# Kernel tuning notes

Measured on AMD Instinct MI355X. Metric: run time of the kernel, lower is better.

The kernel has to match this reference:

```python
import jax, jax.numpy as jnp
import numpy as np

B, S, D, H = 4, 2048, 1024, 16
HD = D // H  # head dim = 64


def setup_inputs() -> dict:
    key = jax.random.key(0)
    ks = jax.random.split(key, 10)
    sd = 1.0 / np.sqrt(D)
    return {
        "x": jax.random.normal(ks[0], (B, S, D), jnp.float32),
        "Wq": jax.random.normal(ks[1], (D, D), jnp.float32) * sd,
        "Wk": jax.random.normal(ks[2], (D, D), jnp.float32) * sd,
        "Wv": jax.random.normal(ks[3], (D, D), jnp.float32) * sd,
        "in_w": jax.random.normal(ks[4], (3 * D, D), jnp.float32) * sd,
        "in_b": jax.random.normal(ks[5], (3 * D,), jnp.float32) * 0.01,
        "out_w": jax.random.normal(ks[6], (D, D), jnp.float32) * sd,
        "out_b": jax.random.normal(ks[7], (D,), jnp.float32) * 0.01,
        "proj_w": jax.random.normal(ks[8], (D, D), jnp.float32) * sd,
        "proj_b": jax.random.normal(ks[9], (D,), jnp.float32) * 0.01,
    }


def _attn_block(x, Wq, Wk, Wv, in_w, in_b, out_w, out_b, proj_w, proj_b):
    b, s, d = x.shape
    # redundant pre-projections (bias-free)
    q = jnp.einsum('bsd,ed->bse', x, Wq)
    k = jnp.einsum('bsd,ed->bse', x, Wk)
    v = jnp.einsum('bsd,ed->bse', x, Wv)
    # MultiheadAttention internal in-projection (with bias)
    wq, wk, wv = in_w[:d], in_w[d:2 * d], in_w[2 * d:]
    bq, bk, bv = in_b[:d], in_b[d:2 * d], in_b[2 * d:]
    Q = jnp.einsum('bse,fe->bsf', q, wq) + bq
    K = jnp.einsum('bse,fe->bsf', k, wk) + bk
    V = jnp.einsum('bse,fe->bsf', v, wv) + bv
    # split heads -> [b, h, s, hd]
    Q = Q.reshape(b, s, H, HD).transpose(0, 2, 1, 3)
    K = K.reshape(b, s, H, HD).transpose(0, 2, 1, 3)
    V = V.reshape(b, s, H, HD).transpose(0, 2, 1, 3)
    scale = 1.0 / np.sqrt(HD)
    scores = jnp.einsum('bhqd,bhkd->bhqk', Q * scale, K)
    # FAITHFUL quirk: float tril mask (ones / zeros) is ADDED to scores,
    # exactly as torch does with a float attn_mask (not a -inf causal mask).
    mask = jnp.tril(jnp.ones((s, s), scores.dtype))
    scores = scores + mask
    A = jax.nn.softmax(scores, axis=-1)
    ctx = jnp.einsum('bhqk,bhkd->bhqd', A, V)
    ctx = ctx.transpose(0, 2, 1, 3).reshape(b, s, d)
    attn = jnp.einsum('bse,fe->bsf', ctx, out_w) + out_b  # out_proj
    out = jnp.einsum('bse,fe->bsf', attn, proj_w) + proj_b  # self.project
    return x + out


def reference(x, Wq, Wk, Wv, in_w, in_b, out_w, out_b, proj_w, proj_b):
    return _attn_block(x, Wq, Wk, Wv, in_w, in_b, out_w, out_b, proj_w, proj_b)
```

## Files before the change

### kernel.cpp

```cpp
#include <hip/hip_runtime.h>
#include <stdint.h>

typedef unsigned short u16;
typedef __attribute__((ext_vector_type(8))) short bfx8;
typedef __attribute__((ext_vector_type(4))) float fx4;
typedef __attribute__((ext_vector_type(16))) float fx16;

static __device__ __forceinline__ u16 f2b(float f) {
  union { float f; uint32_t u; } v; v.f = f;
  uint32_t r = v.u + 0x7fffu + ((v.u >> 16) & 1u);
  return (u16)(r >> 16);
}

static __device__ __forceinline__ uint32_t cvtpk(float lo, float hi) {
  uint32_t r;
  asm("v_cvt_pk_bf16_f32 %0, %1, %2" : "=v"(r) : "v"(lo), "v"(hi));
  return r;
}

static __device__ __forceinline__ float ex2(float x) {
  float r;
  asm("v_exp_f32 %0, %1" : "=v"(r) : "v"(x));
  return r;
}

static __device__ __forceinline__ void gload16(const void* g, void* lds) {
  __builtin_amdgcn_global_load_lds((const __attribute__((address_space(1))) uint32_t*)g,
                                   (__attribute__((address_space(3))) uint32_t*)lds,
                                   16, 0, 0);
}

__global__ __launch_bounds__(256) void f32_to_bf16_k(const float* __restrict__ in,
                                                     u16* __restrict__ out, int n) {
  int i = (blockIdx.x * 256 + threadIdx.x) * 8;
  if (i >= n) return;
  float4 a = *(const float4*)(in + i);
  float4 b = *(const float4*)(in + i + 4);
  bfx8 o;
  o[0]=(short)f2b(a.x); o[1]=(short)f2b(a.y); o[2]=(short)f2b(a.z); o[3]=(short)f2b(a.w);
  o[4]=(short)f2b(b.x); o[5]=(short)f2b(b.y); o[6]=(short)f2b(b.z); o[7]=(short)f2b(b.w);
  *(bfx8*)(out + i) = o;
}

struct TransArgs { const float* in[4]; u16* out[4]; };
__global__ __launch_bounds__(256) void transpose4_k(TransArgs ta) {
  const float* in = ta.in[blockIdx.z];
  u16* out = ta.out[blockIdx.z];
  __shared__ u16 t[64][65];
  const int bx = blockIdx.x * 64, by = blockIdx.y * 64;
  const int tid = threadIdx.x;
#pragma unroll
  for (int i = 0; i < 16; ++i) {
    int idx = tid + i * 256; int r = idx >> 6, c = idx & 63;
    t[c][r] = f2b(in[(size_t)(by + r) * 1024 + bx + c]);
  }
  __syncthreads();
#pragma unroll
  for (int i = 0; i < 16; ++i) {
    int idx = tid + i * 256; int r = idx >> 6, c = idx & 63;
    out[(size_t)(bx + r) * 1024 + by + c] = t[r][c];
  }
}

__global__ __launch_bounds__(256) void make_b2_k(const float* __restrict__ pw,
                                                 const float* __restrict__ ob,
                                                 const float* __restrict__ pb,
                                                 float* __restrict__ b2) {
  const int f = blockIdx.x, tid = threadIdx.x;
  float s = 0.f;
  for (int e = tid; e < 1024; e += 256) s += pw[(size_t)f * 1024 + e] * ob[e];
#pragma unroll
  for (int d = 1; d < 64; d <<= 1) s += __shfl_xor(s, d);
  __shared__ float red[4];
  if ((tid & 63) == 0) red[tid >> 6] = s;
  __syncthreads();
  if (tid == 0) b2[f] = red[0] + red[1] + red[2] + red[3] + pb[f];
}

static __device__ __forceinline__ void gemm_core(const u16* __restrict__ A,
                                                 const u16* __restrict__ Bt,
                                                 int K, int bm, int bn,
                                                 u16* As, u16* Bs, fx4 (&acc)[4][4]) {
  const int tid = threadIdx.x, w = tid >> 6, l = tid & 63, lm = l & 15, lk = l >> 4;
  const int wm = w >> 1, wn = w & 1;
  const int nkt = K >> 6;
  for (int kt = 0; kt < nkt; ++kt) {
#pragma unroll
    for (int i = 0; i < 4; ++i) {
      int off = i * 4096 + w * 1024;
      int loff = off + l * 16;
      int row = loff >> 7, cb = loff & 127;
      gload16((const char*)A + ((size_t)(bm * 128 + row) * K + kt * 64) * 2 + cb,
              (char*)As + off);
      gload16((const char*)Bt + ((size_t)(bn * 128 + row) * K + kt * 64) * 2 + cb,
              (char*)Bs + off);
    }
    __syncthreads();
#pragma unroll
    for (int kk = 0; kk < 2; ++kk) {
      bfx8 a[4], b[4];
#pragma unroll
      for (int mi = 0; mi < 4; ++mi)
        a[mi] = *(const bfx8*)((const char*)As + (wm * 64 + mi * 16 + lm) * 128 + lk * 16 + kk * 64);
#pragma unroll
      for (int nj = 0; nj < 4; ++nj)
        b[nj] = *(const bfx8*)((const char*)Bs + (wn * 64 + nj * 16 + lm) * 128 + lk * 16 + kk * 64);
#pragma unroll
      for (int mi = 0; mi < 4; ++mi)
#pragma unroll
        for (int nj = 0; nj < 4; ++nj)
          acc[mi][nj] = __builtin_amdgcn_mfma_f32_16x16x32_bf16(a[mi], b[nj], acc[mi][nj], 0, 0, 0);
    }
    __syncthreads();
  }
}

struct CombArgs { const u16* A[4]; const u16* Bt[4]; u16* C[4]; };
__global__ __launch_bounds__(256) void gemm_combine_k(CombArgs ca) {
  const int z = blockIdx.z;
  __shared__ u16 As[8192], Bs[8192];
  fx4 acc[4][4];
#pragma unroll
  for (int mi = 0; mi < 4; ++mi)
#pragma unroll
    for (int nj = 0; nj < 4; ++nj) acc[mi][nj] = 0.f;
  gemm_core(ca.A[z], ca.Bt[z], 1024, blockIdx.x, blockIdx.y, As, Bs, acc);
  const int tid = threadIdx.x, w = tid >> 6, l = tid & 63, lm = l & 15, lk = l >> 4;
  const int wm = w >> 1, wn = w & 1;
  u16* C = ca.C[z];
#pragma unroll
  for (int mi = 0; mi < 4; ++mi)
#pragma unroll
    for (int nj = 0; nj < 4; ++nj)
#pragma unroll
      for (int r = 0; r < 4; ++r) {
        int m = blockIdx.x * 128 + wm * 64 + mi * 16 + lk * 4 + r;
        int n = blockIdx.y * 128 + wn * 64 + nj * 16 + lm;
        C[(size_t)m * 1024 + n] = f2b(acc[mi][nj][r]);
      }
}

__global__ __launch_bounds__(256) void gemm_qkv_k(const u16* __restrict__ xb,
                                                  const u16* __restrict__ Wc,
                                                  const float* __restrict__ bias,
                                                  u16* __restrict__ Qh, u16* __restrict__ Kh,
                                                  u16* __restrict__ Vh) {
  __shared__ u16 As[8192], Bs[8192];
  fx4 acc[4][4];
#pragma unroll
  for (int mi = 0; mi < 4; ++mi)
#pragma unroll
    for (int nj = 0; nj < 4; ++nj) acc[mi][nj] = 0.f;
  gemm_core(xb, Wc, 1024, blockIdx.x, blockIdx.y, As, Bs, acc);
  const int tid = threadIdx.x, w = tid >> 6, l = tid & 63, lm = l & 15, lk = l >> 4;
  const int wm = w >> 1, wn = w & 1;
  const int t = (blockIdx.y * 128) >> 10;
  u16* dst = (t == 0) ? Qh : ((t == 1) ? Kh : Vh);
#pragma unroll
  for (int mi = 0; mi < 4; ++mi)
#pragma unroll
    for (int nj = 0; nj < 4; ++nj)
#pragma unroll
      for (int r = 0; r < 4; ++r) {
        int m = blockIdx.x * 128 + wm * 64 + mi * 16 + lk * 4 + r;
        int n = blockIdx.y * 128 + wn * 64 + nj * 16 + lm;
        float v = acc[mi][nj][r] + bias[n];
        int f = n & 1023, h = f >> 6, hd = f & 63, b = m >> 11, s = m & 2047;
        size_t hb = ((size_t)(b * 16 + h)) * 131072;
        size_t idx;
        if (t == 2) {
          int sl = s & 63, st = s >> 6;
          idx = hb + (size_t)st * 4096 + (size_t)(hd * 64 + (sl ^ ((hd & 7) << 3)));
        } else if (t == 1) {
          idx = hb + (size_t)s * 64 + (hd ^ ((s & 7) << 3));
        } else {
          idx = hb + (size_t)s * 64 + hd;
        }
        dst[idx] = f2b(v);
      }
}

__global__ __launch_bounds__(256) void gemm_final_k(const u16* __restrict__ ctx,
                                                    const u16* __restrict__ W2,
                                                    const float* __restrict__ b2,
                                                    const float* __restrict__ x,
                                                    float* __restrict__ out) {
  __shared__ u16 As[8192], Bs[8192];
  fx4 acc[4][4];
#pragma unroll
  for (int mi = 0; mi < 4; ++mi)
#pragma unroll
    for (int nj = 0; nj < 4; ++nj) acc[mi][nj] = 0.f;
  gemm_core(ctx, W2, 1024, blockIdx.x, blockIdx.y, As, Bs, acc);
  const int tid = threadIdx.x, w = tid >> 6, l = tid & 63, lm = l & 15, lk = l >> 4;
  const int wm = w >> 1, wn = w & 1;
#pragma unroll
  for (int mi = 0; mi < 4; ++mi)
#pragma unroll
    for (int nj = 0; nj < 4; ++nj)
#pragma unroll
      for (int r = 0; r < 4; ++r) {
        int m = blockIdx.x * 128 + wm * 64 + mi * 16 + lk * 4 + r;
        int n = blockIdx.y * 128 + wn * 64 + nj * 16 + lm;
        size_t idx = (size_t)m * 1024 + n;
        out[idx] = acc[mi][nj][r] + b2[n] + x[idx];
      }
}

__global__ __launch_bounds__(256, 4) void attn_k(const u16* __restrict__ Qh,
                                                 const u16* __restrict__ Kh,
                                                 const u16* __restrict__ Vh,
                                                 u16* __restrict__ ctx) {
  const int bl = blockIdx.x;
  const int wk = (bl & 7) * 128 + (bl >> 3);
  const int bh = wk >> 4, qt = wk & 15;
  const int tid = threadIdx.x, w = tid >> 6, l = tid & 63;
  const int ql = l & 31, h = l >> 5;
  __shared__ __align__(16) u16 Ks[2][4096];
  __shared__ __align__(16) u16 Vs[2][4096];

  const float SC = 0.18033688011112042f;
  const float MA = 1.4426950408889634f;
  const float THR = 11.541560327111708f;

  const size_t base = (size_t)bh * 131072;
  const int qb = qt * 128 + w * 32;
  const int q = qb + ql;
  bfx8 qf[4];
  {
    const u16* qp = Qh + base + (size_t)q * 64 + 8 * h;
    qf[0] = *(const bfx8*)(qp);
    qf[1] = *(const bfx8*)(qp + 16);
    qf[2] = *(const bfx8*)(qp + 32);
    qf[3] = *(const bfx8*)(qp + 48);
  }
  float m_run = -1024.f, l_part = 0.f;
  fx16 accO[2];
  accO[0] = 0.f; accO[1] = 0.f;

  const char* Kg = (const char*)(Kh + base);
  const char* Vg = (const char*)(Vh + base);
  const int o = tid * 16;
  const int sw8 = (ql & 7) << 4;

#define STAGE(t, s)                                                        \
  {                                                                        \
    gload16(Kg + (size_t)(t) * 8192 + o,        (char*)Ks[s] + o);         \
    gload16(Kg + (size_t)(t) * 8192 + o + 4096, (char*)Ks[s] + o + 4096);  \
    gload16(Vg + (size_t)(t) * 8192 + o,        (char*)Vs[s] + o);         \
    gload16(Vg + (size_t)(t) * 8192 + o + 4096, (char*)Vs[s] + o + 4096);  \
  }

  STAGE(0, 0);
  asm volatile("s_waitcnt vmcnt(0)" ::: "memory");
  __builtin_amdgcn_s_barrier();
  __builtin_amdgcn_sched_barrier(0);

  int cur = 0;
  for (int kt = 0; kt < 32; ++kt) {
    if (kt + 1 < 32) STAGE(kt + 1, cur ^ 1);
    __builtin_amdgcn_sched_barrier(0);

    const char* Kc = (const char*)Ks[cur];
    const char* Vc = (const char*)Vs[cur];

    fx16 sS[2];
    sS[0] = 0.f; sS[1] = 0.f;
    __builtin_amdgcn_s_setprio(1);
#pragma unroll
    for (int ks = 0; ks < 4; ++ks) {
      bfx8 kf0 = *(const bfx8*)(Kc + (0 * 32 + ql) * 128 + (((ks << 5) | (h << 4)) ^ sw8));
      bfx8 kf1 = *(const bfx8*)(Kc + (1 * 32 + ql) * 128 + (((ks << 5) | (h << 4)) ^ sw8));
      sS[0] = __builtin_amdgcn_mfma_f32_32x32x16_bf16(kf0, qf[ks], sS[0], 0, 0, 0);
      sS[1] = __builtin_amdgcn_mfma_f32_32x32x16_bf16(kf1, qf[ks], sS[1], 0, 0, 0);
    }
    __builtin_amdgcn_s_setprio(0);

    const int dk = kt - (qb >> 6);
    {
      float cO = -m_run, cI = cO + MA;
      if (dk < 0) {
#pragma unroll
        for (int r = 0; r < 16; ++r) {
          sS[0][r] = fmaf(sS[0][r], SC, cI);
          sS[1][r] = fmaf(sS[1][r], SC, cI);
        }
      } else if (dk > 0) {
#pragma unroll
        for (int r = 0; r < 16; ++r) {
          sS[0][r] = fmaf(sS[0][r], SC, cO);
          sS[1][r] = fmaf(sS[1][r], SC, cO);
        }
      } else {
#pragma unroll
        for (int kb = 0; kb < 2; ++kb)
#pragma unroll
          for (int r = 0; r < 16; ++r) {
            int key = kt * 64 + kb * 32 + (r & 3) + 8 * (r >> 2) + 4 * h;
            sS[kb][r] = fmaf(sS[kb][r], SC, (key <= q) ? cI : cO);
          }
      }
    }
    float mx;
    {
      float m0 = fmaxf(fmaxf(sS[0][0], sS[0][1]), fmaxf(sS[0][2], sS[0][3]));
      float m1 = fmaxf(fmaxf(sS[0][4], sS[0][5]), fmaxf(sS[0][6], sS[0][7]));
      float m2 = fmaxf(fmaxf(sS[0][8], sS[0][9]), fmaxf(sS[0][10], sS[0][11]));
      float m3 = fmaxf(fmaxf(sS[0][12], sS[0][13]), fmaxf(sS[0][14], sS[0][15]));
      float m4 = fmaxf(fmaxf(sS[1][0], sS[1][1]), fmaxf(sS[1][2], sS[1][3]));
      float m5 = fmaxf(fmaxf(sS[1][4], sS[1][5]), fmaxf(sS[1][6], sS[1][7]));
      float m6 = fmaxf(fmaxf(sS[1][8], sS[1][9]), fmaxf(sS[1][10], sS[1][11]));
      float m7 = fmaxf(fmaxf(sS[1][12], sS[1][13]), fmaxf(sS[1][14], sS[1][15]));
      mx = fmaxf(fmaxf(fmaxf(m0, m1), fmaxf(m2, m3)), fmaxf(fmaxf(m4, m5), fmaxf(m6, m7)));
    }
    float full = fmaxf(mx, __shfl_xor(mx, 32));
    if (!__all(full <= THR)) {
      float d = fmaxf(full, 0.f);
      float corr = ex2(-d);
      m_run += d;
      l_part *= corr;
#pragma unroll
      for (int r = 0; r < 16; ++r) {
        int rq = (r & 3) + 8 * (r >> 2) + 4 * h;
        float cr = __shfl(corr, (l & 32) | rq);
        accO[0][r] *= cr;
        accO[1][r] *= cr;
        sS[0][r] -= d;
        sS[1][r] -= d;
      }
    }
    fx16 tt;
#pragma unroll
    for (int r = 0; r < 16; ++r) {
      sS[0][r] = ex2(sS[0][r]);
      sS[1][r] = ex2(sS[1][r]);
      tt[r] = sS[0][r] + sS[1][r];
    }
    {
      float ls0 = tt[0] + tt[8],  ls1 = tt[1] + tt[9];
      float ls2 = tt[2] + tt[10], ls3 = tt[3] + tt[11];
      float ls4 = tt[4] + tt[12], ls5 = tt[5] + tt[13];
      float ls6 = tt[6] + tt[14], ls7 = tt[7] + tt[15];
      l_part += ((ls0 + ls4) + (ls1 + ls5)) + ((ls2 + ls6) + (ls3 + ls7));
    }
    uint32_t pw[8][2];
#pragma unroll
    for (int kb = 0; kb < 2; ++kb)
#pragma unroll
      for (int gg = 0; gg < 4; ++gg) {
        pw[kb * 4 + gg][0] = cvtpk(sS[kb][4 * gg + 0], sS[kb][4 * gg + 1]);
        pw[kb * 4 + gg][1] = cvtpk(sS[kb][4 * gg + 2], sS[kb][4 * gg + 3]);
      }

    __builtin_amdgcn_s_setprio(1);
#pragma unroll
    for (int ks = 0; ks < 4; ++ks) {
      union { uint32_t u[4]; bfx8 v; } pa;
#pragma unroll
      for (int p = 0; p < 2; ++p) {
        uint32_t contrib = h ? pw[2 * ks][p] : pw[2 * ks + 1][p];
        uint32_t rcv = __shfl_xor(contrib, 32);
        pa.u[p]     = h ? rcv : pw[2 * ks][p];
        pa.u[2 + p] = h ? pw[2 * ks + 1][p] : rcv;
      }
      bfx8 vf0 = *(const bfx8*)(Vc + (0 * 32 + ql) * 128 + (((ks << 5) | (h << 4)) ^ sw8));
      bfx8 vf1 = *(const bfx8*)(Vc + (1 * 32 + ql) * 128 + (((ks << 5) | (h << 4)) ^ sw8));
      accO[0] = __builtin_amdgcn_mfma_f32_32x32x16_bf16(pa.v, vf0, accO[0], 0, 0, 0);
      accO[1] = __builtin_amdgcn_mfma_f32_32x32x16_bf16(pa.v, vf1, accO[1], 0, 0, 0);
    }
    __builtin_amdgcn_s_setprio(0);

    asm volatile("s_waitcnt vmcnt(0)" ::: "memory");
    __builtin_amdgcn_s_barrier();
    __builtin_amdgcn_sched_barrier(0);
    cur ^= 1;
  }
#undef STAGE

  float inv = 1.0f / (l_part + __shfl_xor(l_part, 32));
  const int b = bh >> 4, hcol = bh & 15;
#pragma unroll
  for (int r = 0; r < 16; ++r) {
    int rq = (r & 3) + 8 * (r >> 2) + 4 * h;
    float invq = __shfl(inv, (l & 32) | rq);
    size_t rowb = ((size_t)b * 2048 + (qb + rq)) * 1024 + hcol * 64 + ql;
    ctx[rowb]      = f2b(accO[0][r] * invq);
    ctx[rowb + 32] = f2b(accO[1][r] * invq);
  }
}

extern "C" void kernel_launch(void* const* d_in, const int* in_sizes, int n_in,
                              void* d_out, int out_size, void* d_ws, size_t ws_size,
                              hipStream_t stream) {
  (void)in_sizes; (void)n_in; (void)out_size; (void)ws_size;
  const float* x      = (const float*)d_in[0];
  const float* Wq     = (const float*)d_in[1];
  const float* Wk     = (const float*)d_in[2];
  const float* Wv     = (const float*)d_in[3];
  const float* in_w   = (const float*)d_in[4];
  const float* in_b   = (const float*)d_in[5];
  const float* out_w  = (const float*)d_in[6];
  const float* out_b  = (const float*)d_in[7];
  const float* proj_w = (const float*)d_in[8];
  const float* proj_b = (const float*)d_in[9];
  float* out = (float*)d_out;

  char* ws = (char*)d_ws;
  const size_t MB = 1ull << 20;
  u16* xb   = (u16*)(ws);
  u16* ctx  = xb;
  u16* Qh   = (u16*)(ws + 16 * MB);
  u16* Kh   = (u16*)(ws + 32 * MB);
  u16* Vh   = (u16*)(ws + 48 * MB);
  u16* inwb = Kh;
  u16* tmpT = Vh;
  u16* pwb  = (u16*)(ws + 48 * MB + 8 * MB);
  u16* Wc   = (u16*)(ws + 64 * MB);
  u16* W2   = (u16*)(ws + 70 * MB);
  float* b2 = (float*)(ws + 72 * MB);

  f32_to_bf16_k<<<4096, 256, 0, stream>>>(x, xb, 8388608);
  f32_to_bf16_k<<<1536, 256, 0, stream>>>(in_w, inwb, 3145728);
  f32_to_bf16_k<<<512, 256, 0, stream>>>(proj_w, pwb, 1048576);

  TransArgs ta;
  ta.in[0] = Wq; ta.in[1] = Wk; ta.in[2] = Wv; ta.in[3] = out_w;
  for (int z = 0; z < 4; ++z) ta.out[z] = tmpT + (size_t)z * 1048576;
  transpose4_k<<<dim3(16, 16, 4), 256, 0, stream>>>(ta);

  CombArgs ca;
  ca.A[0] = inwb; ca.A[1] = inwb + 1048576; ca.A[2] = inwb + 2097152; ca.A[3] = pwb;
  for (int z = 0; z < 4; ++z) ca.Bt[z] = tmpT + (size_t)z * 1048576;
  ca.C[0] = Wc; ca.C[1] = Wc + 1048576; ca.C[2] = Wc + 2097152; ca.C[3] = W2;
  gemm_combine_k<<<dim3(8, 8, 4), 256, 0, stream>>>(ca);

  make_b2_k<<<1024, 256, 0, stream>>>(proj_w, out_b, proj_b, b2);

  gemm_qkv_k<<<dim3(64, 24), 256, 0, stream>>>(xb, Wc, in_b, Qh, Kh, Vh);
  attn_k<<<1024, 256, 0, stream>>>(Qh, Kh, Vh, ctx);
  gemm_final_k<<<dim3(64, 8), 256, 0, stream>>>(ctx, W2, b2, x, out);
}
```

Before: 274.6 us.

## Process two 32-row query tiles per wave to reuse K/V fragments

Each wave now handles 64 queries (two 32-row MFMA tiles) instead of 32, so each block covers 256 queries and the grid is halved to 512 blocks. Every K and V fragment read from LDS feeds two MFMAs, and each staged K/V tile is shared across twice as many queries, which halves global K/V traffic and LDS reads per query. The cost is roughly double the accumulator and score registers, so launch bounds drop to 2 blocks per SM, and fewer blocks may hurt load balance and latency hiding.

```diff
diff --git a/kernel.cpp b/kernel.cpp
--- a/kernel.cpp
+++ b/kernel.cpp
@@ -207,13 +207,13 @@
       }
 }
 
-__global__ __launch_bounds__(256, 4) void attn_k(const u16* __restrict__ Qh,
+__global__ __launch_bounds__(256, 2) void attn_k(const u16* __restrict__ Qh,
                                                  const u16* __restrict__ Kh,
                                                  const u16* __restrict__ Vh,
                                                  u16* __restrict__ ctx) {
   const int bl = blockIdx.x;
-  const int wk = (bl & 7) * 128 + (bl >> 3);
-  const int bh = wk >> 4, qt = wk & 15;
+  const int wk = (bl & 7) * 64 + (bl >> 3);
+  const int bh = wk >> 3, qt = wk & 7;
   const int tid = threadIdx.x, w = tid >> 6, l = tid & 63;
   const int ql = l & 31, h = l >> 5;
   __shared__ __align__(16) u16 Ks[2][4096];
@@ -224,19 +224,20 @@
   const float THR = 11.541560327111708f;
 
   const size_t base = (size_t)bh * 131072;
-  const int qb = qt * 128 + w * 32;
-  const int q = qb + ql;
-  bfx8 qf[4];
-  {
-    const u16* qp = Qh + base + (size_t)q * 64 + 8 * h;
-    qf[0] = *(const bfx8*)(qp);
-    qf[1] = *(const bfx8*)(qp + 16);
-    qf[2] = *(const bfx8*)(qp + 32);
-    qf[3] = *(const bfx8*)(qp + 48);
-  }
-  float m_run = -1024.f, l_part = 0.f;
-  fx16 accO[2];
-  accO[0] = 0.f; accO[1] = 0.f;
+  const int qb = qt * 256 + w * 64;
+  bfx8 qf[2][4];
+#pragma unroll
+  for (int j = 0; j < 2; ++j) {
+    const u16* qp = Qh + base + (size_t)(qb + j * 32 + ql) * 64 + 8 * h;
+    qf[j][0] = *(const bfx8*)(qp);
+    qf[j][1] = *(const bfx8*)(qp + 16);
+    qf[j][2] = *(const bfx8*)(qp + 32);
+    qf[j][3] = *(const bfx8*)(qp + 48);
+  }
+  float m_run[2] = {-1024.f, -1024.f};
+  float l_part[2] = {0.f, 0.f};
+  fx16 accO[2][2];
+  accO[0][0] = 0.f; accO[0][1] = 0.f; accO[1][0] = 0.f; accO[1][1] = 0.f;
 
   const char* Kg = (const char*)(Kh + base);
   const char* Vg = (const char*)(Vh + base);
@@ -264,32 +265,37 @@
     const char* Kc = (const char*)Ks[cur];
     const char* Vc = (const char*)Vs[cur];
 
-    fx16 sS[2];
-    sS[0] = 0.f; sS[1] = 0.f;
+    fx16 sS[2][2];
+    sS[0][0] = 0.f; sS[0][1] = 0.f; sS[1][0] = 0.f; sS[1][1] = 0.f;
     __builtin_amdgcn_s_setprio(1);
 #pragma unroll
     for (int ks = 0; ks < 4; ++ks) {
       bfx8 kf0 = *(const bfx8*)(Kc + (0 * 32 + ql) * 128 + (((ks << 5) | (h << 4)) ^ sw8));
       bfx8 kf1 = *(const bfx8*)(Kc + (1 * 32 + ql) * 128 + (((ks << 5) | (h << 4)) ^ sw8));
-      sS[0] = __builtin_amdgcn_mfma_f32_32x32x16_bf16(kf0, qf[ks], sS[0], 0, 0, 0);
-      sS[1] = __builtin_amdgcn_mfma_f32_32x32x16_bf16(kf1, qf[ks], sS[1], 0, 0, 0);
+      sS[0][0] = __builtin_amdgcn_mfma_f32_32x32x16_bf16(kf0, qf[0][ks], sS[0][0], 0, 0, 0);
+      sS[1][0] = __builtin_amdgcn_mfma_f32_32x32x16_bf16(kf0, qf[1][ks], sS[1][0], 0, 0, 0);
+      sS[0][1] = __builtin_amdgcn_mfma_f32_32x32x16_bf16(kf1, qf[0][ks], sS[0][1], 0, 0, 0);
+      sS[1][1] = __builtin_amdgcn_mfma_f32_32x32x16_bf16(kf1, qf[1][ks], sS[1][1], 0, 0, 0);
     }
     __builtin_amdgcn_s_setprio(0);
 
     const int dk = kt - (qb >> 6);
-    {
-      float cO = -m_run, cI = cO + MA;
+    float full[2];
+#pragma unroll
+    for (int j = 0; j < 2; ++j) {
+      const int qj = qb + j * 32 + ql;
+      float cO = -m_run[j], cI = cO + MA;
       if (dk < 0) {
 #pragma unroll
         for (int r = 0; r < 16; ++r) {
-          sS[0][r] = fmaf(sS[0][r], SC, cI);
-          sS[1][r] = fmaf(sS[1][r], SC, cI);
+          sS[j][0][r] = fmaf(sS[j][0][r], SC, cI);
+          sS[j][1][r] = fmaf(sS[j][1][r], SC, cI);
         }
       } else if (dk > 0) {
 #pragma unroll
         for (int r = 0; r < 16; ++r) {
-          sS[0][r] = fmaf(sS[0][r], SC, cO);
-          sS[1][r] = fmaf(sS[1][r], SC, cO);
+          sS[j][0][r] = fmaf(sS[j][0][r], SC, cO);
+          sS[j][1][r] = fmaf(sS[j][1][r], SC, cO);
         }
       } else {
 #pragma unroll
@@ -297,76 +303,80 @@
 #pragma unroll
           for (int r = 0; r < 16; ++r) {
             int key = kt * 64 + kb * 32 + (r & 3) + 8 * (r >> 2) + 4 * h;
-            sS[kb][r] = fmaf(sS[kb][r], SC, (key <= q) ? cI : cO);
+            sS[j][kb][r] = fmaf(sS[j][kb][r], SC, (key <= qj) ? cI : cO);
           }
       }
-    }
-    float mx;
-    {
-      float m0 = fmaxf(fmaxf(sS[0][0], sS[0][1]), fmaxf(sS[0][2], sS[0][3]));
-      float m1 = fmaxf(fmaxf(sS[0][4], sS[0][5]), fmaxf(sS[0][6], sS[0][7]));
-      float m2 = fmaxf(fmaxf(sS[0][8], sS[0][9]), fmaxf(sS[0][10], sS[0][11]));
-      float m3 = fmaxf(fmaxf(sS[0][12], sS[0][13]), fmaxf(sS[0][14], sS[0][15]));
-      float m4 = fmaxf(fmaxf(sS[1][0], sS[1][1]), fmaxf(sS[1][2], sS[1][3]));
-      float m5 = fmaxf(fmaxf(sS[1][4], sS[1][5]), fmaxf(sS[1][6], sS[1][7]));
-      float m6 = fmaxf(fmaxf(sS[1][8], sS[1][9]), fmaxf(sS[1][10], sS[1][11]));
-      float m7 = fmaxf(fmaxf(sS[1][12], sS[1][13]), fmaxf(sS[1][14], sS[1][15]));
-      mx = fmaxf(fmaxf(fmaxf(m0, m1), fmaxf(m2, m3)), fmaxf(fmaxf(m4, m5), fmaxf(m6, m7)));
-    }
-    float full = fmaxf(mx, __shfl_xor(mx, 32));
-    if (!__all(full <= THR)) {
-      float d = fmaxf(full, 0.f);
-      float corr = ex2(-d);
-      m_run += d;
-      l_part *= corr;
+      float m0 = fmaxf(fmaxf(sS[j][0][0], sS[j][0][1]), fmaxf(sS[j][0][2], sS[j][0][3]));
+      float m1 = fmaxf(fmaxf(sS[j][0][4], sS[j][0][5]), fmaxf(sS[j][0][6], sS[j][0][7]));
+      float m2 = fmaxf(fmaxf(sS[j][0][8], sS[j][0][9]), fmaxf(sS[j][0][10], sS[j][0][11]));
+      float m3 = fmaxf(fmaxf(sS[j][0][12], sS[j][0][13]), fmaxf(sS[j][0][14], sS[j][0][15]));
+      float m4 = fmaxf(fmaxf(sS[j][1][0], sS[j][1][1]), fmaxf(sS[j][1][2], sS[j][1][3]));
+      float m5 = fmaxf(fmaxf(sS[j][1][4], sS[j][1][5]), fmaxf(sS[j][1][6], sS[j][1][7]));
+      float m6 = fmaxf(fmaxf(sS[j][1][8], sS[j][1][9]), fmaxf(sS[j][1][10], sS[j][1][11]));
+      float m7 = fmaxf(fmaxf(sS[j][1][12], sS[j][1][13]), fmaxf(sS[j][1][14], sS[j][1][15]));
+      float mx = fmaxf(fmaxf(fmaxf(m0, m1), fmaxf(m2, m3)), fmaxf(fmaxf(m4, m5), fmaxf(m6, m7)));
+      full[j] = fmaxf(mx, __shfl_xor(mx, 32));
+    }
+    if (!__all(fmaxf(full[0], full[1]) <= THR)) {
+#pragma unroll
+      for (int j = 0; j < 2; ++j) {
+        float d = fmaxf(full[j], 0.f);
+        float corr = ex2(-d);
+        m_run[j] += d;
+        l_part[j] *= corr;
+#pragma unroll
+        for (int r = 0; r < 16; ++r) {
+          int rq = (r & 3) + 8 * (r >> 2) + 4 * h;
+          float cr = __shfl(corr, (l & 32) | rq);
+          accO[j][0][r] *= cr;
+          accO[j][1][r] *= cr;
+          sS[j][0][r] -= d;
+          sS[j][1][r] -= d;
+        }
+      }
+    }
+    uint32_t pw[2][8][2];
+#pragma unroll
+    for (int j = 0; j < 2; ++j) {
+      fx16 tt;
 #pragma unroll
       for (int r = 0; r < 16; ++r) {
-        int rq = (r & 3) + 8 * (r >> 2) + 4 * h;
-        float cr = __shfl(corr, (l & 32) | rq);
-        accO[0][r] *= cr;
-        accO[1][r] *= cr;
-        sS[0][r] -= d;
-        sS[1][r] -= d;
-      }
-    }
-    fx16 tt;
-#pragma unroll
-    for (int r = 0; r < 16; ++r) {
-      sS[0][r] = ex2(sS[0][r]);
-      sS[1][r] = ex2(sS[1][r]);
-      tt[r] = sS[0][r] + sS[1][r];
-    }
-    {
+        sS[j][0][r] = ex2(sS[j][0][r]);
+        sS[j][1][r] = ex2(sS[j][1][r]);
+        tt[r] = sS[j][0][r] + sS[j][1][r];
+      }
       float ls0 = tt[0] + tt[8],  ls1 = tt[1] + tt[9];
       float ls2 = tt[2] + tt[10], ls3 = tt[3] + tt[11];
       float ls4 = tt[4] + tt[12], ls5 = tt[5] + tt[13];
       float ls6 = tt[6] + tt[14], ls7 = tt[7] + tt[15];
-      l_part += ((ls0 + ls4) + (ls1 + ls5)) + ((ls2 + ls6) + (ls3 + ls7));
-    }
-    uint32_t pw[8][2];
-#pragma unroll
-    for (int kb = 0; kb < 2; ++kb)
-#pragma unroll
-      for (int gg = 0; gg < 4; ++gg) {
-        pw[kb * 4 + gg][0] = cvtpk(sS[kb][4 * gg + 0], sS[kb][4 * gg + 1]);
-        pw[kb * 4 + gg][1] = cvtpk(sS[kb][4 * gg + 2], sS[kb][4 * gg + 3]);
-      }
+      l_part[j] += ((ls0 + ls4) + (ls1 + ls5)) + ((ls2 + ls6) + (ls3 + ls7));
+#pragma unroll
+      for (int kb = 0; kb < 2; ++kb)
+#pragma unroll
+        for (int gg = 0; gg < 4; ++gg) {
+          pw[j][kb * 4 + gg][0] = cvtpk(sS[j][kb][4 * gg + 0], sS[j][kb][4 * gg + 1]);
+          pw[j][kb * 4 + gg][1] = cvtpk(sS[j][kb][4 * gg + 2], sS[j][kb][4 * gg + 3]);
+        }
+    }
 
     __builtin_amdgcn_s_setprio(1);
 #pragma unroll
     for (int ks = 0; ks < 4; ++ks) {
-      union { uint32_t u[4]; bfx8 v; } pa;
-#pragma unroll
-      for (int p = 0; p < 2; ++p) {
-        uint32_t contrib = h ? pw[2 * ks][p] : pw[2 * ks + 1][p];
-        uint32_t rcv = __shfl_xor(contrib, 32);
-        pa.u[p]     = h ? rcv : pw[2 * ks][p];
-        pa.u[2 + p] = h ? pw[2 * ks + 1][p] : rcv;
-      }
       bfx8 vf0 = *(const bfx8*)(Vc + (0 * 32 + ql) * 128 + (((ks << 5) | (h << 4)) ^ sw8));
       bfx8 vf1 = *(const bfx8*)(Vc + (1 * 32 + ql) * 128 + (((ks << 5) | (h << 4)) ^ sw8));
-      accO[0] = __builtin_amdgcn_mfma_f32_32x32x16_bf16(pa.v, vf0, accO[0], 0, 0, 0);
-      accO[1] = __builtin_amdgcn_mfma_f32_32x32x16_bf16(pa.v, vf1, accO[1], 0, 0, 0);
+#pragma unroll
+      for (int j = 0; j < 2; ++j) {
+        union { uint32_t u[4]; bfx8 v; } pa;
+#pragma unroll
+        for (int p = 0; p < 2; ++p) {
+          uint32_t contrib = h ? pw[j][2 * ks][p] : pw[j][2 * ks + 1][p];
+          uint32_t rcv = __shfl_xor(contrib, 32);
+          pa.u[p]     = h ? rcv : pw[j][2 * ks][p];
+          pa.u[2 + p] = h ? pw[j][2 * ks + 1][p] : rcv;
+        }
+        accO[j][0] = __builtin_amdgcn_mfma_f32_32x32x16_bf16(pa.v, vf0, accO[j][0], 0, 0, 0);
+        accO[j][1] = __builtin_amdgcn_mfma_f32_32x32x16_bf16(pa.v, vf1, accO[j][1], 0, 0, 0);
+      }
     }
     __builtin_amdgcn_s_setprio(0);
 
@@ -377,15 +387,18 @@
   }
 #undef STAGE
 
-  float inv = 1.0f / (l_part + __shfl_xor(l_part, 32));
   const int b = bh >> 4, hcol = bh & 15;
 #pragma unroll
-  for (int r = 0; r < 16; ++r) {
-    int rq = (r & 3) + 8 * (r >> 2) + 4 * h;
-    float invq = __shfl(inv, (l & 32) | rq);
-    size_t rowb = ((size_t)b * 2048 + (qb + rq)) * 1024 + hcol * 64 + ql;
-    ctx[rowb]      = f2b(accO[0][r] * invq);
-    ctx[rowb + 32] = f2b(accO[1][r] * invq);
+  for (int j = 0; j < 2; ++j) {
+    float inv = 1.0f / (l_part[j] + __shfl_xor(l_part[j], 32));
+#pragma unroll
+    for (int r = 0; r < 16; ++r) {
+      int rq = (r & 3) + 8 * (r >> 2) + 4 * h;
+      float invq = __shfl(inv, (l & 32) | rq);
+      size_t rowb = ((size_t)b * 2048 + (qb + j * 32 + rq)) * 1024 + hcol * 64 + ql;
+      ctx[rowb]      = f2b(accO[j][0][r] * invq);
+      ctx[rowb + 32] = f2b(accO[j][1][r] * invq);
+    }
   }
 }
 
@@ -437,6 +450,6 @@
   make_b2_k<<<1024, 256, 0, stream>>>(proj_w, out_b, proj_b, b2);
 
   gemm_qkv_k<<<dim3(64, 24), 256, 0, stream>>>(xb, Wc, in_b, Qh, Kh, Vh);
-  attn_k<<<1024, 256, 0, stream>>>(Qh, Kh, Vh, ctx);
+  attn_k<<<512, 256, 0, stream>>>(Qh, Kh, Vh, ctx);
   gemm_final_k<<<dim3(64, 8), 256, 0, stream>>>(ctx, W2, b2, x, out);
 }
```

Result: slower. 325.7 us (+18.6%).

## Process two 32-row query tiles per warp in attention to reuse K/V fragments

Applied to the files above, without the earlier changes.

Each attention warp now handles 64 query rows as two 32-row sub-tiles, so every K and V fragment read from LDS feeds twice as many MFMAs. Block count halves to 512 with 256 queries per block, and launch bounds drop to one block per CU so the doubled accumulators and Q fragments fit in registers. The aim is to halve LDS traffic and K/V global staging per unit of work. The cost is higher register pressure, lower occupancy and fewer blocks in flight to hide latency.

```diff
diff --git a/kernel.cpp b/kernel.cpp
--- a/kernel.cpp
+++ b/kernel.cpp
@@ -6,6 +6,10 @@
 typedef __attribute__((ext_vector_type(4))) float fx4;
 typedef __attribute__((ext_vector_type(16))) float fx16;
 
+static constexpr float SCc  = 0.18033688011112042f;
+static constexpr float MAc  = 1.4426950408889634f;
+static constexpr float THRc = 11.541560327111708f;
+
 static __device__ __forceinline__ u16 f2b(float f) {
   union { float f; uint32_t u; } v; v.f = f;
   uint32_t r = v.u + 0x7fffu + ((v.u >> 16) & 1u);
@@ -28,6 +32,79 @@
   __builtin_amdgcn_global_load_lds((const __attribute__((address_space(1))) uint32_t*)g,
                                    (__attribute__((address_space(3))) uint32_t*)lds,
                                    16, 0, 0);
+}
+
+static __device__ __forceinline__ void mask_tile(fx16& s, int dk, int kbase4h, int qj,
+                                                 float cO, float cI) {
+  if (dk < 0) {
+#pragma unroll
+    for (int r = 0; r < 16; ++r) s[r] = fmaf(s[r], SCc, cI);
+  } else if (dk > 0) {
+#pragma unroll
+    for (int r = 0; r < 16; ++r) s[r] = fmaf(s[r], SCc, cO);
+  } else {
+#pragma unroll
+    for (int r = 0; r < 16; ++r) {
+      int key = kbase4h + (r & 3) + 8 * (r >> 2);
+      s[r] = fmaf(s[r], SCc, (key <= qj) ? cI : cO);
+    }
+  }
+}
+
+static __device__ __forceinline__ float vmax32(const fx16& a, const fx16& b) {
+  float m0 = fmaxf(fmaxf(a[0], a[1]), fmaxf(a[2], a[3]));
+  float m1 = fmaxf(fmaxf(a[4], a[5]), fmaxf(a[6], a[7]));
+  float m2 = fmaxf(fmaxf(a[8], a[9]), fmaxf(a[10], a[11]));
+  float m3 = fmaxf(fmaxf(a[12], a[13]), fmaxf(a[14], a[15]));
+  float m4 = fmaxf(fmaxf(b[0], b[1]), fmaxf(b[2], b[3]));
+  float m5 = fmaxf(fmaxf(b[4], b[5]), fmaxf(b[6], b[7]));
+  float m6 = fmaxf(fmaxf(b[8], b[9]), fmaxf(b[10], b[11]));
+  float m7 = fmaxf(fmaxf(b[12], b[13]), fmaxf(b[14], b[15]));
+  return fmaxf(fmaxf(fmaxf(m0, m1), fmaxf(m2, m3)), fmaxf(fmaxf(m4, m5), fmaxf(m6, m7)));
+}
+
+static __device__ __forceinline__ void rescale32(fx16& o0, fx16& o1, fx16& s0, fx16& s1,
+                                                 float d, float corr, int lane, int h) {
+#pragma unroll
+  for (int r = 0; r < 16; ++r) {
+    int rq = (r & 3) + 8 * (r >> 2) + 4 * h;
+    float cr = __shfl(corr, (lane & 32) | rq);
+    o0[r] *= cr; o1[r] *= cr; s0[r] -= d; s1[r] -= d;
+  }
+}
+
+static __device__ __forceinline__ float expsum32(fx16& s0, fx16& s1) {
+  fx16 tt;
+#pragma unroll
+  for (int r = 0; r < 16; ++r) { s0[r] = ex2(s0[r]); s1[r] = ex2(s1[r]); tt[r] = s0[r] + s1[r]; }
+  float a0 = tt[0] + tt[8],  a1 = tt[1] + tt[9];
+  float a2 = tt[2] + tt[10], a3 = tt[3] + tt[11];
+  float a4 = tt[4] + tt[12], a5 = tt[5] + tt[13];
+  float a6 = tt[6] + tt[14], a7 = tt[7] + tt[15];
+  return ((a0 + a4) + (a1 + a5)) + ((a2 + a6) + (a3 + a7));
+}
+
+static __device__ __forceinline__ void pack32(const fx16& s0, const fx16& s1,
+                                              uint32_t (&pw)[8][2]) {
+#pragma unroll
+  for (int gg = 0; gg < 4; ++gg) {
+    pw[gg][0]     = cvtpk(s0[4 * gg + 0], s0[4 * gg + 1]);
+    pw[gg][1]     = cvtpk(s0[4 * gg + 2], s0[4 * gg + 3]);
+    pw[4 + gg][0] = cvtpk(s1[4 * gg + 0], s1[4 * gg + 1]);
+    pw[4 + gg][1] = cvtpk(s1[4 * gg + 2], s1[4 * gg + 3]);
+  }
+}
+
+static __device__ __forceinline__ bfx8 mk_pa(const uint32_t (&pw)[8][2], int ks, int h) {
+  union { uint32_t u[4]; bfx8 v; } pa;
+#pragma unroll
+  for (int p = 0; p < 2; ++p) {
+    uint32_t contrib = h ? pw[2 * ks][p] : pw[2 * ks + 1][p];
+    uint32_t rcv = __shfl_xor(contrib, 32);
+    pa.u[p]     = h ? rcv : pw[2 * ks][p];
+    pa.u[2 + p] = h ? pw[2 * ks + 1][p] : rcv;
+  }
+  return pa.v;
 }
 
 __global__ __launch_bounds__(256) void f32_to_bf16_k(const float* __restrict__ in,
@@ -207,36 +284,32 @@
       }
 }
 
-__global__ __launch_bounds__(256, 4) void attn_k(const u16* __restrict__ Qh,
+__global__ __launch_bounds__(256, 1) void attn_k(const u16* __restrict__ Qh,
                                                  const u16* __restrict__ Kh,
                                                  const u16* __restrict__ Vh,
                                                  u16* __restrict__ ctx) {
   const int bl = blockIdx.x;
-  const int wk = (bl & 7) * 128 + (bl >> 3);
-  const int bh = wk >> 4, qt = wk & 15;
+  const int wk = (bl & 7) * 64 + (bl >> 3);
+  const int bh = wk >> 3, qt = wk & 7;
   const int tid = threadIdx.x, w = tid >> 6, l = tid & 63;
   const int ql = l & 31, h = l >> 5;
   __shared__ __align__(16) u16 Ks[2][4096];
   __shared__ __align__(16) u16 Vs[2][4096];
 
-  const float SC = 0.18033688011112042f;
-  const float MA = 1.4426950408889634f;
-  const float THR = 11.541560327111708f;
-
   const size_t base = (size_t)bh * 131072;
-  const int qb = qt * 128 + w * 32;
-  const int q = qb + ql;
-  bfx8 qf[4];
+  const int qb = qt * 256 + w * 64;
+  const int qA = qb + ql, qB = qb + 32 + ql;
+  bfx8 qfA[4], qfB[4];
   {
-    const u16* qp = Qh + base + (size_t)q * 64 + 8 * h;
-    qf[0] = *(const bfx8*)(qp);
-    qf[1] = *(const bfx8*)(qp + 16);
-    qf[2] = *(const bfx8*)(qp + 32);
-    qf[3] = *(const bfx8*)(qp + 48);
-  }
-  float m_run = -1024.f, l_part = 0.f;
-  fx16 accO[2];
-  accO[0] = 0.f; accO[1] = 0.f;
+    const u16* qp = Qh + base + (size_t)qA * 64 + 8 * h;
+    qfA[0] = *(const bfx8*)(qp);      qfA[1] = *(const bfx8*)(qp + 16);
+    qfA[2] = *(const bfx8*)(qp + 32); qfA[3] = *(const bfx8*)(qp + 48);
+    const u16* qp2 = Qh + base + (size_t)qB * 64 + 8 * h;
+    qfB[0] = *(const bfx8*)(qp2);      qfB[1] = *(const bfx8*)(qp2 + 16);
+    qfB[2] = *(const bfx8*)(qp2 + 32); qfB[3] = *(const bfx8*)(qp2 + 48);
+  }
+  float mA = -1024.f, mB = -1024.f, lA = 0.f, lB = 0.f;
+  fx16 accA0 = 0.f, accA1 = 0.f, accB0 = 0.f, accB1 = 0.f;
 
   const char* Kg = (const char*)(Kh + base);
   const char* Vg = (const char*)(Vh + base);
@@ -264,109 +337,59 @@
     const char* Kc = (const char*)Ks[cur];
     const char* Vc = (const char*)Vs[cur];
 
-    fx16 sS[2];
-    sS[0] = 0.f; sS[1] = 0.f;
+    fx16 sA0 = 0.f, sA1 = 0.f, sB0 = 0.f, sB1 = 0.f;
     __builtin_amdgcn_s_setprio(1);
 #pragma unroll
     for (int ks = 0; ks < 4; ++ks) {
       bfx8 kf0 = *(const bfx8*)(Kc + (0 * 32 + ql) * 128 + (((ks << 5) | (h << 4)) ^ sw8));
       bfx8 kf1 = *(const bfx8*)(Kc + (1 * 32 + ql) * 128 + (((ks << 5) | (h << 4)) ^ sw8));
-      sS[0] = __builtin_amdgcn_mfma_f32_32x32x16_bf16(kf0, qf[ks], sS[0], 0, 0, 0);
-      sS[1] = __builtin_amdgcn_mfma_f32_32x32x16_bf16(kf1, qf[ks], sS[1], 0, 0, 0);
+      sA0 = __builtin_amdgcn_mfma_f32_32x32x16_bf16(kf0, qfA[ks], sA0, 0, 0, 0);
+      sB0 = __builtin_amdgcn_mfma_f32_32x32x16_bf16(kf0, qfB[ks], sB0, 0, 0, 0);
+      sA1 = __builtin_amdgcn_mfma_f32_32x32x16_bf16(kf1, qfA[ks], sA1, 0, 0, 0);
+      sB1 = __builtin_amdgcn_mfma_f32_32x32x16_bf16(kf1, qfB[ks], sB1, 0, 0, 0);
     }
     __builtin_amdgcn_s_setprio(0);
 
     const int dk = kt - (qb >> 6);
     {
-      float cO = -m_run, cI = cO + MA;
-      if (dk < 0) {
-#pragma unroll
-        for (int r = 0; r < 16; ++r) {
-          sS[0][r] = fmaf(sS[0][r], SC, cI);
-          sS[1][r] = fmaf(sS[1][r], SC, cI);
-        }
-      } else if (dk > 0) {
-#pragma unroll
-        for (int r = 0; r < 16; ++r) {
-          sS[0][r] = fmaf(sS[0][r], SC, cO);
-          sS[1][r] = fmaf(sS[1][r], SC, cO);
-        }
-      } else {
-#pragma unroll
-        for (int kb = 0; kb < 2; ++kb)
-#pragma unroll
-          for (int r = 0; r < 16; ++r) {
-            int key = kt * 64 + kb * 32 + (r & 3) + 8 * (r >> 2) + 4 * h;
-            sS[kb][r] = fmaf(sS[kb][r], SC, (key <= q) ? cI : cO);
-          }
-      }
-    }
-    float mx;
+      float cO = -mA, cI = cO + MAc;
+      mask_tile(sA0, dk, kt * 64 + 4 * h,      qA, cO, cI);
+      mask_tile(sA1, dk, kt * 64 + 32 + 4 * h, qA, cO, cI);
+    }
     {
-      float m0 = fmaxf(fmaxf(sS[0][0], sS[0][1]), fmaxf(sS[0][2], sS[0][3]));
-      float m1 = fmaxf(fmaxf(sS[0][4], sS[0][5]), fmaxf(sS[0][6], sS[0][7]));
-      float m2 = fmaxf(fmaxf(sS[0][8], sS[0][9]), fmaxf(sS[0][10], sS[0][11]));
-      float m3 = fmaxf(fmaxf(sS[0][12], sS[0][13]), fmaxf(sS[0][14], sS[0][15]));
-      float m4 = fmaxf(fmaxf(sS[1][0], sS[1][1]), fmaxf(sS[1][2], sS[1][3]));
-      float m5 = fmaxf(fmaxf(sS[1][4], sS[1][5]), fmaxf(sS[1][6], sS[1][7]));
-      float m6 = fmaxf(fmaxf(sS[1][8], sS[1][9]), fmaxf(sS[1][10], sS[1][11]));
-      float m7 = fmaxf(fmaxf(sS[1][12], sS[1][13]), fmaxf(sS[1][14], sS[1][15]));
-      mx = fmaxf(fmaxf(fmaxf(m0, m1), fmaxf(m2, m3)), fmaxf(fmaxf(m4, m5), fmaxf(m6, m7)));
-    }
-    float full = fmaxf(mx, __shfl_xor(mx, 32));
-    if (!__all(full <= THR)) {
-      float d = fmaxf(full, 0.f);
-      float corr = ex2(-d);
-      m_run += d;
-      l_part *= corr;
-#pragma unroll
-      for (int r = 0; r < 16; ++r) {
-        int rq = (r & 3) + 8 * (r >> 2) + 4 * h;
-        float cr = __shfl(corr, (l & 32) | rq);
-        accO[0][r] *= cr;
-        accO[1][r] *= cr;
-        sS[0][r] -= d;
-        sS[1][r] -= d;
-      }
-    }
-    fx16 tt;
-#pragma unroll
-    for (int r = 0; r < 16; ++r) {
-      sS[0][r] = ex2(sS[0][r]);
-      sS[1][r] = ex2(sS[1][r]);
-      tt[r] = sS[0][r] + sS[1][r];
-    }
-    {
-      float ls0 = tt[0] + tt[8],  ls1 = tt[1] + tt[9];
-      float ls2 = tt[2] + tt[10], ls3 = tt[3] + tt[11];
-      float ls4 = tt[4] + tt[12], ls5 = tt[5] + tt[13];
-      float ls6 = tt[6] + tt[14], ls7 = tt[7] + tt[15];
-      l_part += ((ls0 + ls4) + (ls1 + ls5)) + ((ls2 + ls6) + (ls3 + ls7));
-    }
-    uint32_t pw[8][2];
-#pragma unroll
-    for (int kb = 0; kb < 2; ++kb)
-#pragma unroll
-      for (int gg = 0; gg < 4; ++gg) {
-        pw[kb * 4 + gg][0] = cvtpk(sS[kb][4 * gg + 0], sS[kb][4 * gg + 1]);
-        pw[kb * 4 + gg][1] = cvtpk(sS[kb][4 * gg + 2], sS[kb][4 * gg + 3]);
-      }
+      float cO = -mB, cI = cO + MAc;
+      mask_tile(sB0, dk, kt * 64 + 4 * h,      qB, cO, cI);
+      mask_tile(sB1, dk, kt * 64 + 32 + 4 * h, qB, cO, cI);
+    }
+    float mxA = vmax32(sA0, sA1);
+    float mxB = vmax32(sB0, sB1);
+    float fullA = fmaxf(mxA, __shfl_xor(mxA, 32));
+    float fullB = fmaxf(mxB, __shfl_xor(mxB, 32));
+    if (!__all(fmaxf(fullA, fullB) <= THRc)) {
+      float dA = fmaxf(fullA, 0.f), corrA = ex2(-dA);
+      mA += dA; lA *= corrA;
+      rescale32(accA0, accA1, sA0, sA1, dA, corrA, l, h);
+      float dB = fmaxf(fullB, 0.f), corrB = ex2(-dB);
+      mB += dB; lB *= corrB;
+      rescale32(accB0, accB1, sB0, sB1, dB, corrB, l, h);
+    }
+    lA += expsum32(sA0, sA1);
+    lB += expsum32(sB0, sB1);
+    uint32_t pwA[8][2], pwB[8][2];
+    pack32(sA0, sA1, pwA);
+    pack32(sB0, sB1, pwB);
 
     __builtin_amdgcn_s_setprio(1);
 #pragma unroll
     for (int ks = 0; ks < 4; ++ks) {
-      union { uint32_t u[4]; bfx8 v; } pa;
-#pragma unroll
-      for (int p = 0; p < 2; ++p) {
-        uint32_t contrib = h ? pw[2 * ks][p] : pw[2 * ks + 1][p];
-        uint32_t rcv = __shfl_xor(contrib, 32);
-        pa.u[p]     = h ? rcv : pw[2 * ks][p];
-        pa.u[2 + p] = h ? pw[2 * ks + 1][p] : rcv;
-      }
       bfx8 vf0 = *(const bfx8*)(Vc + (0 * 32 + ql) * 128 + (((ks << 5) | (h << 4)) ^ sw8));
       bfx8 vf1 = *(const bfx8*)(Vc + (1 * 32 + ql) * 128 + (((ks << 5) | (h << 4)) ^ sw8));
-      accO[0] = __builtin_amdgcn_mfma_f32_32x32x16_bf16(pa.v, vf0, accO[0], 0, 0, 0);
-      accO[1] = __builtin_amdgcn_mfma_f32_32x32x16_bf16(pa.v, vf1, accO[1], 0, 0, 0);
+      bfx8 paA = mk_pa(pwA, ks, h);
+      bfx8 paB = mk_pa(pwB, ks, h);
+      accA0 = __builtin_amdgcn_mfma_f32_32x32x16_bf16(paA, vf0, accA0, 0, 0, 0);
+      accB0 = __builtin_amdgcn_mfma_f32_32x32x16_bf16(paB, vf0, accB0, 0, 0, 0);
+      accA1 = __builtin_amdgcn_mfma_f32_32x32x16_bf16(paA, vf1, accA1, 0, 0, 0);
+      accB1 = __builtin_amdgcn_mfma_f32_32x32x16_bf16(paB, vf1, accB1, 0, 0, 0);
     }
     __builtin_amdgcn_s_setprio(0);
 
@@ -377,15 +400,28 @@
   }
 #undef STAGE
 
-  float inv = 1.0f / (l_part + __shfl_xor(l_part, 32));
   const int b = bh >> 4, hcol = bh & 15;
-#pragma unroll
-  for (int r = 0; r < 16; ++r) {
-    int rq = (r & 3) + 8 * (r >> 2) + 4 * h;
-    float invq = __shfl(inv, (l & 32) | rq);
-    size_t rowb = ((size_t)b * 2048 + (qb + rq)) * 1024 + hcol * 64 + ql;
-    ctx[rowb]      = f2b(accO[0][r] * invq);
-    ctx[rowb + 32] = f2b(accO[1][r] * invq);
+  {
+    float inv = 1.0f / (lA + __shfl_xor(lA, 32));
+#pragma unroll
+    for (int r = 0; r < 16; ++r) {
+      int rq = (r & 3) + 8 * (r >> 2) + 4 * h;
+      float invq = __shfl(inv, (l & 32) | rq);
+      size_t rowb = ((size_t)b * 2048 + (qb + rq)) * 1024 + hcol * 64 + ql;
+      ctx[rowb]      = f2b(accA0[r] * invq);
+      ctx[rowb + 32] = f2b(accA1[r] * invq);
+    }
+  }
+  {
+    float inv = 1.0f / (lB + __shfl_xor(lB, 32));
+#pragma unroll
+    for (int r = 0; r < 16; ++r) {
+      int rq = (r & 3) + 8 * (r >> 2) + 4 * h;
+      float invq = __shfl(inv, (l & 32) | rq);
+      size_t rowb = ((size_t)b * 2048 + (qb + 32 + rq)) * 1024 + hcol * 64 + ql;
+      ctx[rowb]      = f2b(accB0[r] * invq);
+      ctx[rowb + 32] = f2b(accB1[r] * invq);
+    }
   }
 }
 
@@ -437,6 +473,6 @@
   make_b2_k<<<1024, 256, 0, stream>>>(proj_w, out_b, proj_b, b2);
 
   gemm_qkv_k<<<dim3(64, 24), 256, 0, stream>>>(xb, Wc, in_b, Qh, Kh, Vh);
-  attn_k<<<1024, 256, 0, stream>>>(Qh, Kh, Vh, ctx);
+  attn_k<<<512, 256, 0, stream>>>(Qh, Kh, Vh, ctx);
   gemm_final_k<<<dim3(64, 8), 256, 0, stream>>>(ctx, W2, b2, x, out);
 }
```

New measurement: 316.8 us. 1.15x slower.
